# Kernel optimization log

Measured on AMD Instinct MI355X. Metric: run time of the kernel, lower is better.

The kernel has to match this reference:

```python
import jax, jax.numpy as jnp
import numpy as np

N, E, F_IN, F_E, H = 50000, 800000, 128, 16, 64
NEG_SLOPE = 0.2


def _glorot(key, shape):
    fan_in, fan_out = shape[0], shape[-1]
    lim = np.sqrt(6.0 / (fan_in + fan_out))
    return jax.random.uniform(key, shape, jnp.float32, -lim, lim)


def setup_inputs() -> dict:
    key = jax.random.key(0)
    ks = jax.random.split(key, 24)
    inp = {
        "x": jax.random.normal(ks[0], (N, F_IN), jnp.float32),
        "edge_index": jax.random.randint(ks[1], (2, E), 0, N, jnp.int64),
        "edge_attr": jax.random.normal(ks[2], (E, F_E), jnp.float32),
    }
    k = 3
    for i, f_in in zip((1, 2, 3), (F_IN, H, H)):
        inp[f"W{i}"] = _glorot(ks[k], (f_in, H)); k += 1
        inp[f"as{i}"] = _glorot(ks[k], (H,)); k += 1
        inp[f"ad{i}"] = _glorot(ks[k], (H,)); k += 1
        inp[f"We{i}"] = _glorot(ks[k], (F_E, H)); k += 1
        inp[f"ae{i}"] = _glorot(ks[k], (H,)); k += 1
        inp[f"b{i}"] = jnp.zeros((H,), jnp.float32)
        k += 1
    return inp


def gat_conv(x, src, dst, ea, W, a_s, a_d, We, a_e, b):
    # x: [N, f_in]; src/dst: [E'] (self-loops already appended); ea: [E', F_E]
    n = x.shape[0]
    h = x @ W                                   # [N, H]
    alpha_src = h @ a_s                          # [N]
    alpha_dst = h @ a_d                          # [N]
    alpha_e = (ea @ We) @ a_e                    # [E']
    alpha = alpha_src[src] + alpha_dst[dst] + alpha_e
    alpha = jnp.where(alpha > 0, alpha, NEG_SLOPE * alpha)  # leaky_relu
    # segment softmax over incoming edges of each dst node
    amax = jax.ops.segment_max(alpha, dst, num_segments=n)
    ex = jnp.exp(alpha - amax[dst])
    denom = jax.ops.segment_sum(ex, dst, num_segments=n)
    coef = ex / (denom[dst] + 1e-16)             # [E']
    out = jax.ops.segment_sum(h[src] * coef[:, None], dst, num_segments=n)
    return out + b


def reference(x, edge_index, edge_attr,
              W1, as1, ad1, We1, ae1, b1,
              W2, as2, ad2, We2, ae2, b2,
              W3, as3, ad3, We3, ae3, b3):
    n = x.shape[0]
    # add self-loops (PyG GATConv default), edge_attr fill_value='mean'
    loop = jnp.arange(n, dtype=edge_index.dtype)
    src = jnp.concatenate([edge_index[0], loop])
    dst = jnp.concatenate([edge_index[1], loop])
    ea_mean = jnp.mean(edge_attr, axis=0)
    ea = jnp.concatenate([edge_attr, jnp.broadcast_to(ea_mean, (n, edge_attr.shape[1]))], axis=0)

    x1 = jax.nn.elu(gat_conv(x, src, dst, ea, W1, as1, ad1, We1, ae1, b1))
    x2 = jax.nn.elu(gat_conv(x1, src, dst, ea, W2, as2, ad2, We2, ae2, b2))
    x3 = jax.nn.elu(gat_conv(x2, src, dst, ea, W3, as3, ad3, We3, ae3, b3))
    node_embeddings = x1 + x2 + x3
    graph_embedding = jnp.mean(node_embeddings, axis=0, keepdims=True)  # batch=None path
    return node_embeddings, graph_embedding
```

## Files before the change

### kernel.cpp

```cpp
#include <hip/hip_runtime.h>
#include <hip/hip_fp16.h>
#include <math.h>

#define HD 64
#define MAXNBK 512

typedef unsigned long long u64;
typedef _Float16 f16;
typedef _Float16 f16x8 __attribute__((ext_vector_type(8)));
typedef float f32x4 __attribute__((ext_vector_type(4)));

__device__ __forceinline__ u64 pack_rec(int src, float a0, float a1, float a2) {
    return (u64)(src & 0xFFFF)
         | ((u64)__half_as_ushort(__float2half(a0)) << 16)
         | ((u64)__half_as_ushort(__float2half(a1)) << 32)
         | ((u64)__half_as_ushort(__float2half(a2)) << 48);
}

__global__ void k_init(int* bcnt, float* gacc, int* tick, float* suG,
                       const float* We1, const float* ae1,
                       const float* We2, const float* ae2,
                       const float* We3, const float* ae3, int FE) {
    int t = threadIdx.x;
    for (int i = t; i < MAXNBK; i += 256) bcnt[i] = 0;
    if (t < HD) gacc[t] = 0.f;
    if (t == 0) *tick = 0;
    if (t < 3 * FE) {
        int l = t / FE, f = t % FE;
        const float* We = (l == 0) ? We1 : (l == 1) ? We2 : We3;
        const float* ae = (l == 0) ? ae1 : (l == 1) ? ae2 : ae3;
        float s = 0.f;
        for (int hh = 0; hh < HD; ++hh) s += We[f * HD + hh] * ae[hh];
        suG[t] = s;
    }
}

__global__ void k_pre(const int* __restrict__ ei, const float* __restrict__ ea,
                      const float* __restrict__ suG,
                      int E, int FE, u64* __restrict__ recE,
                      float* __restrict__ partials,
                      int ntiles, int chunk, int* bcnt, int NBK) {
    extern __shared__ float lds[];
    int t = threadIdx.x;

    if (blockIdx.x >= ntiles) {
        int* lc = (int*)lds;
        for (int i = t; i < NBK; i += 256) lc[i] = 0;
        __syncthreads();
        int cb = blockIdx.x - ntiles;
        int lo = cb * chunk, hi = min(E, lo + chunk);
        for (int e = lo + t; e < hi; e += 256)
            atomicAdd(&lc[ei[E + e] >> 7], 1);
        __syncthreads();
        for (int i = t; i < NBK; i += 256)
            if (lc[i]) atomicAdd(&bcnt[i], lc[i]);
        return;
    }

    float* sEA = lds;
    float* su = sEA + 256 * (FE + 1);
    float* colacc = su + 3 * FE;
    int ldE = FE + 1;

    if (t < 3 * FE) su[t] = suG[t];

    const float4* ea4 = (const float4*)ea;
    size_t tot4 = (size_t)E * FE / 4;
    int per_tile4 = 64 * FE;
    size_t base4 = (size_t)blockIdx.x * per_tile4;
    float4 acc = make_float4(0.f, 0.f, 0.f, 0.f);
    for (int i = t; i < per_tile4; i += 256) {
        size_t g4 = base4 + i;
        if (g4 < tot4) {
            float4 v = ea4[g4];
            acc.x += v.x; acc.y += v.y; acc.z += v.z; acc.w += v.w;
            int g = i * 4;
            int e_loc = g / FE, f = g % FE;
            float* p = &sEA[e_loc * ldE + f];
            p[0] = v.x; p[1] = v.y; p[2] = v.z; p[3] = v.w;
        }
    }
    colacc[t * 4 + 0] = acc.x; colacc[t * 4 + 1] = acc.y;
    colacc[t * 4 + 2] = acc.z; colacc[t * 4 + 3] = acc.w;
    __syncthreads();

    int e = blockIdx.x * 256 + t;
    if (e < E) {
        float a0 = 0.f, a1 = 0.f, a2 = 0.f;
        const float* row = &sEA[t * ldE];
        for (int f = 0; f < FE; ++f) {
            float v = row[f];
            a0 += v * su[f];
            a1 += v * su[FE + f];
            a2 += v * su[2 * FE + f];
        }
        int src = ei[e];
        recE[e] = pack_rec(src, a0, a1, a2);
    }
    if (t < 16) {
        int q = t >> 2, j = t & 3;
        float s = 0.f;
        for (int k = 0; k < 64; ++k) s += colacc[(q + k * 4) * 4 + j];
        partials[blockIdx.x * 16 + (q * 4 + j)] = s;
    }
}

__global__ void k_u2(const float* __restrict__ partials, int NB,
                     const float* __restrict__ suG,
                     float* sE, int FE, float invE,
                     const int* __restrict__ bcnt,
                     int* bfill , int* bbase, int NBK, int E) {
    __shared__ float red[256 * 4];
    __shared__ float mea[16];
    __shared__ int ib[256];
    int t = threadIdx.x;
    const float4* p4 = (const float4*)partials;
    int tot4 = NB * 4;
    float4 acc = make_float4(0.f, 0.f, 0.f, 0.f);
    for (int i = t; i < tot4; i += 256) {
        float4 v = p4[i];
        acc.x += v.x; acc.y += v.y; acc.z += v.z; acc.w += v.w;
    }
    red[t * 4 + 0] = acc.x; red[t * 4 + 1] = acc.y;
    red[t * 4 + 2] = acc.z; red[t * 4 + 3] = acc.w;
    int i0 = 2 * t, i1 = 2 * t + 1;
    int c0 = (i0 < NBK) ? bcnt[i0] : 0;
    int c1 = (i1 < NBK) ? bcnt[i1] : 0;
    ib[t] = c0 + c1;
    __syncthreads();
    for (int d = 1; d < 256; d <<= 1) {
        int x = (t >= d) ? ib[t - d] : 0;
        __syncthreads();
        ib[t] += x;
        __syncthreads();
    }
    int excl = ib[t] - (c0 + c1);
    if (i0 < NBK) { bbase[i0] = excl;      bfill[i0 * 16] = excl; }
    if (i1 < NBK) { bbase[i1] = excl + c0; bfill[i1 * 16] = excl + c0; }
    if (t == 0) bbase[NBK] = E;
    if (t < 16) {
        int q = t >> 2, j = t & 3;
        float s = 0.f;
        for (int k = 0; k < 64; ++k) s += red[(q + k * 4) * 4 + j];
        mea[q * 4 + j] = s * invE;
    }
    __syncthreads();
    if (t < 3) {
        float a = 0.f;
        for (int f = 0; f < FE; ++f) a += mea[f] * suG[t * FE + f];
        sE[t] = a;
    }
}

__global__ void k_bucket(const int* __restrict__ ei, const u64* __restrict__ recE,
                         int E, int chunk, int* bfill ,
                         u64* __restrict__ binned, unsigned char* __restrict__ bdstl,
                         int NBK) {
    __shared__ int lcnt[MAXNBK], gb[MAXNBK], lrank[MAXNBK];
    int t = threadIdx.x;
    for (int i = t; i < NBK; i += 256) lcnt[i] = 0;
    __syncthreads();
    int lo = blockIdx.x * chunk, hi = min(E, lo + chunk);
    for (int e = lo + t; e < hi; e += 256)
        atomicAdd(&lcnt[ei[E + e] >> 7], 1);
    __syncthreads();
    for (int i = t; i < NBK; i += 256) {
        lrank[i] = 0;
        gb[i] = lcnt[i] ? atomicAdd(&bfill[i * 16], lcnt[i]) : 0;
    }
    __syncthreads();
    for (int e = lo + t; e < hi; e += 256) {
        u64 r = recE[e];
        int dst = ei[E + e];
        int b = dst >> 7;
        int rank = atomicAdd(&lrank[b], 1);
        int pos = gb[b] + rank;
        binned[pos] = r;
        bdstl[pos] = (unsigned char)(dst & 127);
    }
}

__global__ void k_sort(const int* __restrict__ bbase, const u64* __restrict__ binned,
                       const unsigned char* __restrict__ bdstl,
                       const float* __restrict__ sE,
                       int* __restrict__ row_ptr,
                       u64* __restrict__ rec, int N, int E) {
    __shared__ int lcnt[128], lfill[128];
    int b = blockIdx.x, t = threadIdx.x;
    int base = bbase[b], nrec = bbase[b + 1] - base;
    if (t < 128) lcnt[t] = 0;
    __syncthreads();
    for (int i = t; i < nrec; i += 256)
        atomicAdd(&lcnt[bdstl[base + i]], 1);
    __syncthreads();
    int v = (t < 128) ? lcnt[t] : 0;
    for (int d = 1; d < 128; d <<= 1) {
        int x = (t >= d && t < 128) ? lcnt[t - d] : 0;
        __syncthreads();
        if (t < 128) lcnt[t] += x;
        __syncthreads();
    }
    int gnode = (b << 7) + t;
    if (t < 128) {
        int rp = base + gnode + (lcnt[t] - v);
        if (gnode < N) {
            row_ptr[gnode] = rp;
            rec[rp] = pack_rec(gnode, sE[0], sE[1], sE[2]);
        }
        lfill[t] = rp + 1;
    }
    if (b == 0 && t == 0) row_ptr[N] = E + N;
    __syncthreads();
    for (int i = t; i < nrec; i += 256) {
        u64 r = binned[base + i];
        int dl = bdstl[base + i];
        int p = atomicAdd(&lfill[dl], 1);
        rec[p] = r;
    }
}

__global__ void k_gemm(const void* __restrict__ xin, int in_f16,
                       const float* __restrict__ W,
                       const float* __restrict__ a_s, const float* __restrict__ a_d,
                       __half* __restrict__ h, float* __restrict__ as_n,
                       float* __restrict__ ad_n, int N, int K) {
    extern __shared__ char smem[];
    const int SK = K + 8;
    f16* xs = (f16*)smem;
    f16* wt = xs + 64 * SK;
    int t = threadIdx.x;
    int nb = blockIdx.x * 64;

    int nK4 = K >> 2;
    if (in_f16) {
        const __half* xh = (const __half*)xin;
        for (int i = t; i < 64 * nK4; i += 256) {
            int row = i / nK4, c4 = i % nK4;
            int gr = nb + row; if (gr >= N) gr = N - 1;
            u64 v = ((const u64*)(xh + (size_t)gr * K))[c4];
            *(u64*)&xs[row * SK + c4 * 4] = v;
        }
    } else {
        const float* xf = (const float*)xin;
        for (int i = t; i < 64 * nK4; i += 256) {
            int row = i / nK4, c4 = i % nK4;
            int gr = nb + row; if (gr >= N) gr = N - 1;
            float4 v = ((const float4*)(xf + (size_t)gr * K))[c4];
            f16* p = &xs[row * SK + c4 * 4];
            p[0] = (f16)v.x; p[1] = (f16)v.y; p[2] = (f16)v.z; p[3] = (f16)v.w;
        }
    }
    for (int i = t; i < K * 64; i += 256) {
        int k = i >> 6, c = i & 63;
        wt[c * SK + k] = (f16)W[i];
    }
    __syncthreads();

    int wv = t >> 6, lane = t & 63;
    int m = lane & 15, quad = lane >> 4;
    int rowA = wv * 16 + m;

    f32x4 acc[4];
#pragma unroll
    for (int ct = 0; ct < 4; ++ct) acc[ct] = (f32x4){0.f, 0.f, 0.f, 0.f};

    for (int ks = 0; ks < (K >> 5); ++ks) {
        f16x8 a = *(const f16x8*)&xs[rowA * SK + ks * 32 + quad * 8];
#pragma unroll
        for (int ct = 0; ct < 4; ++ct) {
            f16x8 bf = *(const f16x8*)&wt[(ct * 16 + m) * SK + ks * 32 + quad * 8];
            acc[ct] = __builtin_amdgcn_mfma_f32_16x16x32_f16(a, bf, acc[ct], 0, 0, 0);
        }
    }

    {
        float as_c[4], ad_c[4];
#pragma unroll
        for (int ct = 0; ct < 4; ++ct) {
            as_c[ct] = a_s[ct * 16 + m];
            ad_c[ct] = a_d[ct * 16 + m];
        }
#pragma unroll
        for (int r = 0; r < 4; ++r) {
            float ps = acc[0][r] * as_c[0] + acc[1][r] * as_c[1]
                     + acc[2][r] * as_c[2] + acc[3][r] * as_c[3];
            float pd = acc[0][r] * ad_c[0] + acc[1][r] * ad_c[1]
                     + acc[2][r] * ad_c[2] + acc[3][r] * ad_c[3];
#pragma unroll
            for (int dd = 8; dd; dd >>= 1) {
                ps += __shfl_xor(ps, dd, 64);
                pd += __shfl_xor(pd, dd, 64);
            }
            if (m == 0) {
                int gr = nb + wv * 16 + quad * 4 + r;
                if (gr < N) { as_n[gr] = ps; ad_n[gr] = pd; }
            }
        }
    }

    __syncthreads();
    f16* ht = xs;
    const int HS = 72;
#pragma unroll
    for (int ct = 0; ct < 4; ++ct)
#pragma unroll
        for (int r = 0; r < 4; ++r) {
            int rl = wv * 16 + quad * 4 + r;
            ht[rl * HS + ct * 16 + m] = (f16)acc[ct][r];
        }
    __syncthreads();

    {
        int row = t >> 2, cb = (t & 3) * 16;
        int gr = nb + row;
        if (gr < N) {
            ulonglong2 v0 = *(const ulonglong2*)&ht[row * HS + cb];
            ulonglong2 v1 = *(const ulonglong2*)&ht[row * HS + cb + 8];
            *(ulonglong2*)(h + (size_t)gr * HD + cb) = v0;
            *(ulonglong2*)(h + (size_t)gr * HD + cb + 8) = v1;
        }
    }
}

__global__ void k_aggr(const __half* __restrict__ h, const float* __restrict__ as_n,
                       const float* __restrict__ ad_n, const int* __restrict__ row_ptr,
                       const u64* __restrict__ rec, int l,
                       const float* __restrict__ b, __half* __restrict__ x_out,
                       float* __restrict__ emb, int N, int first) {
    int wave = threadIdx.x >> 6, lane = threadIdx.x & 63;
    int n = blockIdx.x * 4 + wave;
    if (n >= N) return;
    int base = row_ptr[n], end = row_ptr[n + 1];
    float adv = ad_n[n];
    const int shift = 16 * (l + 1);
    int qq = lane >> 3, fo = lane & 7;
    float m = -INFINITY, d = 0.f;
    float acc[8];
#pragma unroll
    for (int k = 0; k < 8; ++k) acc[k] = 0.f;

    for (int c = base; c < end; c += 64) {
        int cnt = min(64, end - c);
        float a = -INFINITY;
        int s = 0;
        if (lane < cnt) {
            u64 r = rec[c + lane];
            s = (int)(r & 0xFFFFull);
            float aE = __half2float(__ushort_as_half((unsigned short)(r >> shift)));
            a = as_n[s] + adv + aE;
            a = (a > 0.f) ? a : 0.2f * a;
        }
        float mc = a;
#pragma unroll
        for (int dd = 32; dd; dd >>= 1) mc = fmaxf(mc, __shfl_xor(mc, dd, 64));
        float mn = fmaxf(m, mc);
        float w = (lane < cnt) ? __expf(a - mn) : 0.f;
        float dc = w;
#pragma unroll
        for (int dd = 32; dd; dd >>= 1) dc += __shfl_xor(dc, dd, 64);
        float sc = __expf(m - mn);
        d = d * sc + dc;
#pragma unroll
        for (int k = 0; k < 8; ++k) acc[k] *= sc;
        m = mn;
        int iters = (cnt + 7) >> 3;
        for (int j8 = 0; j8 < iters; ++j8) {
            int j = (j8 << 3) + qq;
            int sj = __shfl(s, j, 64);
            float wj = __shfl(w, j, 64);
            uint4 hv = *(const uint4*)(h + (size_t)sj * HD + (fo << 3));
            asm("v_fma_mix_f32 %0, %1, %2, %0 op_sel:[0,0,0] op_sel_hi:[0,1,0]"
                : "+v"(acc[0]) : "v"(wj), "v"(hv.x));
            asm("v_fma_mix_f32 %0, %1, %2, %0 op_sel:[0,1,0] op_sel_hi:[0,1,0]"
                : "+v"(acc[1]) : "v"(wj), "v"(hv.x));
            asm("v_fma_mix_f32 %0, %1, %2, %0 op_sel:[0,0,0] op_sel_hi:[0,1,0]"
                : "+v"(acc[2]) : "v"(wj), "v"(hv.y));
            asm("v_fma_mix_f32 %0, %1, %2, %0 op_sel:[0,1,0] op_sel_hi:[0,1,0]"
                : "+v"(acc[3]) : "v"(wj), "v"(hv.y));
            asm("v_fma_mix_f32 %0, %1, %2, %0 op_sel:[0,0,0] op_sel_hi:[0,1,0]"
                : "+v"(acc[4]) : "v"(wj), "v"(hv.z));
            asm("v_fma_mix_f32 %0, %1, %2, %0 op_sel:[0,1,0] op_sel_hi:[0,1,0]"
                : "+v"(acc[5]) : "v"(wj), "v"(hv.z));
            asm("v_fma_mix_f32 %0, %1, %2, %0 op_sel:[0,0,0] op_sel_hi:[0,1,0]"
                : "+v"(acc[6]) : "v"(wj), "v"(hv.w));
            asm("v_fma_mix_f32 %0, %1, %2, %0 op_sel:[0,1,0] op_sel_hi:[0,1,0]"
                : "+v"(acc[7]) : "v"(wj), "v"(hv.w));
        }
    }

#pragma unroll
    for (int k = 0; k < 8; ++k) {
        acc[k] += __shfl_xor(acc[k], 8, 64);
        acc[k] += __shfl_xor(acc[k], 16, 64);
        acc[k] += __shfl_xor(acc[k], 32, 64);
    }
    if (qq == 0) {
        float inv = 1.f / (d + 1e-16f);
        const float4* b4p = (const float4*)(b + (fo << 3));
        float4 b0 = b4p[0], b1 = b4p[1];
        float bb[8] = {b0.x, b0.y, b0.z, b0.w, b1.x, b1.y, b1.z, b1.w};
        float vv[8];
#pragma unroll
        for (int k = 0; k < 8; ++k) {
            float v = acc[k] * inv + bb[k];
            vv[k] = (v > 0.f) ? v : expm1f(v);
        }
        union { unsigned short us[8]; ulonglong2 u2; } ou;
#pragma unroll
        for (int k = 0; k < 8; ++k) ou.us[k] = __half_as_ushort(__float2half(vv[k]));
        *(ulonglong2*)(x_out + (size_t)n * HD + (fo << 3)) = ou.u2;
        float4* ep = (float4*)(emb + (size_t)n * HD + (fo << 3));
        if (first) {
            ep[0] = make_float4(vv[0], vv[1], vv[2], vv[3]);
            ep[1] = make_float4(vv[4], vv[5], vv[6], vv[7]);
        } else {
            float4 e0 = ep[0], e1 = ep[1];
            e0.x += vv[0]; e0.y += vv[1]; e0.z += vv[2]; e0.w += vv[3];
            e1.x += vv[4]; e1.y += vv[5]; e1.z += vv[6]; e1.w += vv[7];
            ep[0] = e0; ep[1] = e1;
        }
    }
}

__global__ void k_red(float* __restrict__ emb, float* __restrict__ gacc,
                      int* __restrict__ tick, int N) {
    __shared__ float lds[256];
    __shared__ int lastf;
    int f = threadIdx.x & 63, w = threadIdx.x >> 6;
    float s = 0.f;
    for (int n = blockIdx.x * 4 + w; n < N; n += gridDim.x * 4)
        s += emb[(size_t)n * HD + f];
    lds[threadIdx.x] = s;
    __syncthreads();
    if (w == 0) {
        float v = lds[f] + lds[64 + f] + lds[128 + f] + lds[192 + f];
        atomicAdd(&gacc[f], v);
    }
    __syncthreads();
    __threadfence();
    if (threadIdx.x == 0)
        lastf = (atomicAdd(tick, 1) == (int)gridDim.x - 1);
    __syncthreads();
    if (lastf && threadIdx.x < HD) {
        float g = __hip_atomic_load(&gacc[threadIdx.x], __ATOMIC_RELAXED,
                                    __HIP_MEMORY_SCOPE_AGENT);
        emb[(size_t)N * HD + threadIdx.x] = g / (float)N;
    }
}

extern "C" void kernel_launch(void* const* d_in, const int* in_sizes, int n_in,
                              void* d_out, int out_size, void* d_ws, size_t ws_size,
                              hipStream_t stream) {
    const float* x = (const float*)d_in[0];
    const int* ei = (const int*)d_in[1];
    const float* ea = (const float*)d_in[2];

    const int FIN = in_sizes[3] / HD;
    const int N = in_sizes[0] / FIN;
    const int E = in_sizes[1] / 2;
    const int FE = in_sizes[2] / E;
    const int NBK = (N + 127) >> 7;
    const int NPRE = 512;

    const float* W[3];  const float* as_[3]; const float* ad_[3];
    const float* We[3]; const float* ae_[3]; const float* bb[3];
    for (int l = 0; l < 3; ++l) {
        W[l]  = (const float*)d_in[3 + 6 * l + 0];
        as_[l] = (const float*)d_in[3 + 6 * l + 1];
        ad_[l] = (const float*)d_in[3 + 6 * l + 2];
        We[l] = (const float*)d_in[3 + 6 * l + 3];
        ae_[l] = (const float*)d_in[3 + 6 * l + 4];
        bb[l] = (const float*)d_in[3 + 6 * l + 5];
    }

    int ntiles = (E + 255) / 256;
    int chunk = (E + NPRE - 1) / NPRE;

    char* ws = (char*)d_ws;
    size_t off = 0;
    auto alloc = [&](size_t bytes) {
        void* p = ws + off;
        off += (bytes + 255) & ~(size_t)255;
        return p;
    };
    __half* h      = (__half*)alloc((size_t)N * HD * 2);
    __half* x_cur  = (__half*)alloc((size_t)N * HD * 2);
    float*  as_n   = (float*)alloc((size_t)N * 4);
    float*  ad_n   = (float*)alloc((size_t)N * 4);
    int*    rowp   = (int*)alloc((size_t)(N + 1) * 4);
    int*    bcnt   = (int*)alloc((size_t)MAXNBK * 4);
    int*    bfill  = (int*)alloc((size_t)MAXNBK * 16 * 4);
    int*    bbase  = (int*)alloc((size_t)(MAXNBK + 1) * 4);
    u64*    rec    = (u64*)alloc((size_t)(E + N) * 8);
    u64*    recE   = (u64*)alloc((size_t)E * 8);
    u64*    binned = (u64*)alloc((size_t)E * 8);
    unsigned char* bdstl = (unsigned char*)alloc((size_t)E);
    float*  partials = (float*)alloc((size_t)ntiles * 16 * 4);
    float*  sE     = (float*)alloc(3 * 4);
    float*  gacc   = (float*)alloc(HD * 4);
    float*  suG    = (float*)alloc(3 * 16 * 4);
    int*    tick   = (int*)alloc(4);
    (void)ws_size; (void)n_in; (void)out_size;

    float* emb = (float*)d_out;

    k_init<<<1, 256, 0, stream>>>(bcnt, gacc, tick, suG,
                                  We[0], ae_[0], We[1], ae_[1], We[2], ae_[2], FE);
    size_t pre_lds = (size_t)(256 * (FE + 1) + 3 * FE + 256 * 4) * 4;
    k_pre<<<ntiles + NPRE, 256, pre_lds, stream>>>(ei, ea, suG, E, FE, recE, partials,
                                                   ntiles, chunk, bcnt, NBK);
    k_u2<<<1, 256, 0, stream>>>(partials, ntiles, suG, sE, FE, 1.0f / (float)E,
                                bcnt, bfill, bbase, NBK, E);
    k_bucket<<<NPRE, 256, 0, stream>>>(ei, recE, E, chunk, bfill, binned, bdstl, NBK);
    k_sort<<<NBK, 256, 0, stream>>>(bbase, binned, bdstl, sE, rowp, rec, N, E);

    for (int l = 0; l < 3; ++l) {
        const void* xin = (l == 0) ? (const void*)x : (const void*)x_cur;
        int in_f16 = (l == 0) ? 0 : 1;
        int K = (l == 0) ? FIN : HD;
        size_t ldsz = (size_t)(2 * 64 * (K + 8)) * 2;
        k_gemm<<<(N + 63) / 64, 256, ldsz, stream>>>(xin, in_f16, W[l], as_[l], ad_[l],
                                                     h, as_n, ad_n, N, K);
        k_aggr<<<(N + 3) / 4, 256, 0, stream>>>(h, as_n, ad_n, rowp, rec, l,
                                                bb[l], x_cur, emb, N, (l == 0) ? 1 : 0);
    }

    k_red<<<256, 256, 0, stream>>>(emb, gacc, tick, N);
}
```

Measured before the change: 384.1 us.

## Process two destination nodes per wave in GAT aggregation kernel

The aggregation kernel now gives each half-wave (32 lanes) its own destination node, so each 64-lane wave handles two nodes. Edge chunks shrink from 64 to 32, and the reductions and shuffles are confined to the half-wave. Each gather iteration covers 4 edges per node instead of 8. This targets wasted lanes on low-degree nodes, at the cost of divergence when the two nodes in a wave have different degrees.

```diff
diff --git a/kernel.cpp b/kernel.cpp
--- a/kernel.cpp
+++ b/kernel.cpp
@@ -328,23 +328,27 @@
                        const float* __restrict__ b, __half* __restrict__ x_out,
                        float* __restrict__ emb, int N, int first) {
     int wave = threadIdx.x >> 6, lane = threadIdx.x & 63;
-    int n = blockIdx.x * 4 + wave;
-    if (n >= N) return;
-    int base = row_ptr[n], end = row_ptr[n + 1];
-    float adv = ad_n[n];
+    int hl = lane & 31;
+    int n = blockIdx.x * 8 + wave * 2 + (lane >> 5);
+    int nc = min(n, N - 1);
+    int base = row_ptr[nc], end = row_ptr[nc + 1];
+    float adv = ad_n[nc];
     const int shift = 16 * (l + 1);
-    int qq = lane >> 3, fo = lane & 7;
+    int qq = (lane >> 3) & 3, fo = lane & 7;
+    int nch = (end - base + 31) >> 5;
+    int nchmax = max(nch, __shfl_xor(nch, 32, 64));
     float m = -INFINITY, d = 0.f;
     float acc[8];
 #pragma unroll
     for (int k = 0; k < 8; ++k) acc[k] = 0.f;
 
-    for (int c = base; c < end; c += 64) {
-        int cnt = min(64, end - c);
+    for (int ch = 0; ch < nchmax; ++ch) {
+        int c = base + (ch << 5);
+        int cnt = min(32, end - c);
         float a = -INFINITY;
         int s = 0;
-        if (lane < cnt) {
-            u64 r = rec[c + lane];
+        if (hl < cnt) {
+            u64 r = rec[c + hl];
             s = (int)(r & 0xFFFFull);
             float aE = __half2float(__ushort_as_half((unsigned short)(r >> shift)));
             a = as_n[s] + adv + aE;
@@ -352,22 +356,23 @@
         }
         float mc = a;
 #pragma unroll
-        for (int dd = 32; dd; dd >>= 1) mc = fmaxf(mc, __shfl_xor(mc, dd, 64));
+        for (int dd = 16; dd; dd >>= 1) mc = fmaxf(mc, __shfl_xor(mc, dd, 64));
         float mn = fmaxf(m, mc);
-        float w = (lane < cnt) ? __expf(a - mn) : 0.f;
+        float w = (hl < cnt) ? __expf(a - mn) : 0.f;
         float dc = w;
 #pragma unroll
-        for (int dd = 32; dd; dd >>= 1) dc += __shfl_xor(dc, dd, 64);
+        for (int dd = 16; dd; dd >>= 1) dc += __shfl_xor(dc, dd, 64);
         float sc = __expf(m - mn);
         d = d * sc + dc;
 #pragma unroll
         for (int k = 0; k < 8; ++k) acc[k] *= sc;
         m = mn;
-        int iters = (cnt + 7) >> 3;
-        for (int j8 = 0; j8 < iters; ++j8) {
-            int j = (j8 << 3) + qq;
-            int sj = __shfl(s, j, 64);
-            float wj = __shfl(w, j, 64);
+        int iters = (max(cnt, 0) + 3) >> 2;
+        for (int j4 = 0; j4 < iters; ++j4) {
+            int j = (j4 << 2) + qq;
+            int sl = (lane & 32) + j;
+            int sj = __shfl(s, sl, 64);
+            float wj = __shfl(w, sl, 64);
             uint4 hv = *(const uint4*)(h + (size_t)sj * HD + (fo << 3));
             asm("v_fma_mix_f32 %0, %1, %2, %0 op_sel:[0,0,0] op_sel_hi:[0,1,0]"
                 : "+v"(acc[0]) : "v"(wj), "v"(hv.x));
@@ -392,9 +397,8 @@
     for (int k = 0; k < 8; ++k) {
         acc[k] += __shfl_xor(acc[k], 8, 64);
         acc[k] += __shfl_xor(acc[k], 16, 64);
-        acc[k] += __shfl_xor(acc[k], 32, 64);
-    }
-    if (qq == 0) {
+    }
+    if (hl < 8 && n < N) {
         float inv = 1.f / (d + 1e-16f);
         const float4* b4p = (const float4*)(b + (fo << 3));
         float4 b0 = b4p[0], b1 = b4p[1];
@@ -521,7 +525,7 @@
         size_t ldsz = (size_t)(2 * 64 * (K + 8)) * 2;
         k_gemm<<<(N + 63) / 64, 256, ldsz, stream>>>(xin, in_f16, W[l], as_[l], ad_[l],
                                                      h, as_n, ad_n, N, K);
-        k_aggr<<<(N + 3) / 4, 256, 0, stream>>>(h, as_n, ad_n, rowp, rec, l,
+        k_aggr<<<(N + 7) / 8, 256, 0, stream>>>(h, as_n, ad_n, rowp, rec, l,
                                                 bb[l], x_cur, emb, N, (l == 0) ? 1 : 0);
     }
 
```

New measurement: 355.2 us. 1.08x faster.
